# Kernel optimization log

Hardware: AMD Instinct MI355X
Metric: run time of the kernel (lower is better)

The kernel has to match this reference:

```python
import jax, jax.numpy as jnp
import numpy as np

# ---- module constants (from init_kwargs) ----
S = 524288            # number of env states (batch)
N_OBJ = 8             # 1 agent + 7 enemies
N_PROP = 6
AGENT_IDX = np.array([0])
ENEMY_IDX = np.array([1, 2, 3, 4, 5, 6, 7])
TYPE_OBJ = [AGENT_IDX, ENEMY_IDX]          # obj_type_indices per type name
TYPE_CODES = [(0, 1), (1, 0)]              # passed_obj_combs
PROP_CODES = np.array([0, 1])              # props
P_SATISFIED = np.array([True, True])       # p_satisfactions
EXIST_THRESH = 0.8


def setup_inputs() -> dict:
    key = jax.random.key(0)
    k1, = jax.random.split(key, 1)
    x = jax.random.uniform(k1, (S, N_OBJ, N_PROP), dtype=jnp.float32)
    action = jnp.array([1.0, 0.0, 1.0], dtype=jnp.float32)      # action_type
    mask = jnp.array([True, False])                              # action_mask
    pred_bounds = jnp.array([[0.0, 0.5], [0.1, 0.9]], dtype=jnp.float32)  # per-pred [min,max]
    return {"x": x, "action": action, "mask": mask, "pred_bounds": pred_bounds}


def _check_exists(x, mask):
    # faithful to check_exists: x[:, obj_type_indices, obj_indices] > 0.8, prod over objs
    agent_exist = jnp.all(x[:, AGENT_IDX, 0] > EXIST_THRESH, axis=-1)   # (S,)
    enemy_exist = jnp.all(x[:, ENEMY_IDX, 1] > EXIST_THRESH, axis=-1)   # (S,)
    obj_type_exists = jnp.stack([agent_exist, enemy_exist], axis=1)      # (S, 2)
    return jnp.all(mask[None, :] == obj_type_exists, axis=1)            # (S,)


def reference(x, action, mask, pred_bounds):
    exist_satisfy = _check_exists(x, mask)                 # (S,)
    action_norm = action / (action + 1e-20)                # value written to satisfied rows
    p_flags = jnp.asarray(P_SATISFIED)                     # (npred,)
    ap_list, pv_list = [], []
    for (t1, t2) in TYPE_CODES:
        o1, o2 = TYPE_OBJ[t1], TYPE_OBJ[t2]
        o1g, o2g = np.meshgrid(o1, o2, indexing="ij")      # all (obj_1, obj_2) pairs
        o1f, o2f = o1g.reshape(-1), o2g.reshape(-1)        # (P,)
        A = x[:, o1f[:, None], PROP_CODES[None, :]]        # (S, P, nprop)
        B = x[:, o2f[:, None], PROP_CODES[None, :]]
        d = jnp.abs(A - B)[..., None]                      # (S, P, nprop, 1)
        # pred.eval: within [min, max] parameter bound; p_values = evaluated distance
        sat = (d >= pred_bounds[:, 0]) & (d <= pred_bounds[:, 1])   # (S, P, nprop, npred)
        sat = jnp.where(p_flags, sat, True)                # unsatisfied preds -> all-true
        pv = jnp.where(p_flags, jnp.broadcast_to(d, sat.shape), 0.0)
        comb_sat = jnp.all(sat, axis=-1)                   # prod over preds   (S, P, nprop)
        satisfies = jnp.any(comb_sat, axis=(1, 2)) & exist_satisfy   # bool += then *= exist
        ap = jnp.where(satisfies[:, None], action_norm[None, :], 0.0)  # (S, n_actions)
        ap_list.append(ap)
        # p_spaces list order: obj pair -> prop -> pred, each entry (1, S)
        pv_list.append(jnp.transpose(pv, (1, 2, 3, 0)).reshape(-1, x.shape[0]))
    action_probs = jnp.stack(ap_list)   # (n_combs, S, n_actions)
    p_values = jnp.stack(pv_list)       # (n_combs, P*nprop*npred, S)
    return (action_probs, p_values)
```

## Files before the change

kernel.cpp:

```cpp
#include <hip/hip_runtime.h>


__global__ __launch_bounds__(256) void ump_kernel(
    const float* __restrict__ x,
    const float* __restrict__ action,
    const unsigned char* __restrict__ mask,
    const float* __restrict__ pred_bounds,
    float* __restrict__ out, int S)
{
    int s = blockIdx.x * blockDim.x + threadIdx.x;
    if (s >= S) return;

    const float* row = x + (size_t)s * 48;

    float2 a = *(const float2*)(row);

    const float lo0 = pred_bounds[0], hi0 = pred_bounds[1];
    const float lo1 = pred_bounds[2], hi1 = pred_bounds[3];

    float d[14];
    bool enemy_all = true;
    bool any_sat = false;
#pragma unroll
    for (int i = 0; i < 7; ++i) {
        float2 b = *(const float2*)(row + (i + 1) * 6);
        enemy_all = enemy_all && (b.y > 0.8f);
        float d0 = fabsf(a.x - b.x);
        float d1 = fabsf(a.y - b.y);
        d[2 * i]     = d0;
        d[2 * i + 1] = d1;
        bool s0 = (d0 >= lo0) && (d0 <= hi0) && (d0 >= lo1) && (d0 <= hi1);
        bool s1 = (d1 >= lo0) && (d1 <= hi0) && (d1 >= lo1) && (d1 <= hi1);
        any_sat = any_sat || s0 || s1;
    }

    bool agent_exist = a.x > 0.8f;
    bool m0 = mask[0] != 0;
    bool m1 = mask[1] != 0;
    bool exist     = (m0 == agent_exist) && (m1 == enemy_all);
    bool satisfies = exist && any_sat;

    float an0 = action[0] / (action[0] + 1e-20f);
    float an1 = action[1] / (action[1] + 1e-20f);
    float an2 = action[2] / (action[2] + 1e-20f);
    float v0 = satisfies ? an0 : 0.0f;
    float v1 = satisfies ? an1 : 0.0f;
    float v2 = satisfies ? an2 : 0.0f;

    size_t sl = (size_t)s;
    size_t Sl = (size_t)S;

    float* ap0 = out + sl * 3;
    ap0[0] = v0; ap0[1] = v1; ap0[2] = v2;
    float* ap1 = out + Sl * 3 + sl * 3;
    ap1[0] = v0; ap1[1] = v1; ap1[2] = v2;

    float* q = out + Sl * 6 + sl;
#pragma unroll
    for (int t = 0; t < 2; ++t) {
#pragma unroll
        for (int i = 0; i < 7; ++i) {
#pragma unroll
            for (int p = 0; p < 2; ++p) {
                float val = d[2 * i + p];
                q[0] = val; q += Sl;
                q[0] = val; q += Sl;
            }
        }
    }
}

extern "C" void kernel_launch(void* const* d_in, const int* in_sizes, int n_in,
                              void* d_out, int out_size, void* d_ws, size_t ws_size,
                              hipStream_t stream) {
    const float*         x           = (const float*)d_in[0];
    const float*         action      = (const float*)d_in[1];
    const unsigned char* mask        = (const unsigned char*)d_in[2];
    const float*         pred_bounds = (const float*)d_in[3];
    float* out = (float*)d_out;

    const int S = in_sizes[0] / 48;
    const int block = 256;
    const int grid = (S + block - 1) / block;
    ump_kernel<<<grid, block, 0, stream>>>(x, action, mask, pred_bounds, out, S);
}
```

Baseline: 214.7 us.

## Process four states per thread with vectorized nontemporal output stores

Each thread now handles four consecutive states, so the per-state distance values can be written as 128-bit vector stores along the S dimension, and the action-prob rows as 16-byte vector stores. All output stores use nontemporal hints to avoid cache pollution. The change cuts the number of store instructions, but input reads become strided across four rows per thread and the thread count drops by four, which lowers occupancy and latency hiding. It also assumes S is a multiple of 4.

```diff
diff --git a/kernel.cpp b/kernel.cpp
--- a/kernel.cpp
+++ b/kernel.cpp
@@ -1,5 +1,7 @@
 #include <hip/hip_runtime.h>
 
+
+typedef float v4f __attribute__((ext_vector_type(4)));
 
 __global__ __launch_bounds__(256) void ump_kernel(
     const float* __restrict__ x,
@@ -8,65 +10,83 @@
     const float* __restrict__ pred_bounds,
     float* __restrict__ out, int S)
 {
-    int s = blockIdx.x * blockDim.x + threadIdx.x;
-    if (s >= S) return;
+    int t = blockIdx.x * blockDim.x + threadIdx.x;
+    int s0 = t * 4;
+    if (s0 >= S) return;
 
-    const float* row = x + (size_t)s * 48;
-
-    float2 a = *(const float2*)(row);
+    const size_t Sl = (size_t)S;
+    const float* row0 = x + (size_t)s0 * 48;
 
     const float lo0 = pred_bounds[0], hi0 = pred_bounds[1];
     const float lo1 = pred_bounds[2], hi1 = pred_bounds[3];
 
-    float d[14];
-    bool enemy_all = true;
-    bool any_sat = false;
+    float2 a[4];
+#pragma unroll
+    for (int r = 0; r < 4; ++r)
+        a[r] = *(const float2*)(row0 + r * 48);
+
+    bool enemy_all[4] = {true, true, true, true};
+    bool any_sat[4]   = {false, false, false, false};
+
+    float* pv = out + Sl * 6 + s0;
+
 #pragma unroll
     for (int i = 0; i < 7; ++i) {
-        float2 b = *(const float2*)(row + (i + 1) * 6);
-        enemy_all = enemy_all && (b.y > 0.8f);
-        float d0 = fabsf(a.x - b.x);
-        float d1 = fabsf(a.y - b.y);
-        d[2 * i]     = d0;
-        d[2 * i + 1] = d1;
-        bool s0 = (d0 >= lo0) && (d0 <= hi0) && (d0 >= lo1) && (d0 <= hi1);
-        bool s1 = (d1 >= lo0) && (d1 <= hi0) && (d1 >= lo1) && (d1 <= hi1);
-        any_sat = any_sat || s0 || s1;
+        float2 b[4];
+#pragma unroll
+        for (int r = 0; r < 4; ++r)
+            b[r] = *(const float2*)(row0 + r * 48 + (i + 1) * 6);
+
+        v4f d0, d1;
+#pragma unroll
+        for (int r = 0; r < 4; ++r) {
+            float e0 = fabsf(a[r].x - b[r].x);
+            float e1 = fabsf(a[r].y - b[r].y);
+            d0[r] = e0;
+            d1[r] = e1;
+            enemy_all[r] = enemy_all[r] && (b[r].y > 0.8f);
+            bool s0b = (e0 >= lo0) && (e0 <= hi0) && (e0 >= lo1) && (e0 <= hi1);
+            bool s1b = (e1 >= lo0) && (e1 <= hi0) && (e1 >= lo1) && (e1 <= hi1);
+            any_sat[r] = any_sat[r] || s0b || s1b;
+        }
+
+        float* q = pv + (size_t)(4 * i) * Sl;
+        __builtin_nontemporal_store(d0, (v4f*)(q));
+        __builtin_nontemporal_store(d0, (v4f*)(q + Sl));
+        __builtin_nontemporal_store(d1, (v4f*)(q + 2 * Sl));
+        __builtin_nontemporal_store(d1, (v4f*)(q + 3 * Sl));
+        float* q2 = q + 28 * Sl;
+        __builtin_nontemporal_store(d0, (v4f*)(q2));
+        __builtin_nontemporal_store(d0, (v4f*)(q2 + Sl));
+        __builtin_nontemporal_store(d1, (v4f*)(q2 + 2 * Sl));
+        __builtin_nontemporal_store(d1, (v4f*)(q2 + 3 * Sl));
     }
 
-    bool agent_exist = a.x > 0.8f;
     bool m0 = mask[0] != 0;
     bool m1 = mask[1] != 0;
-    bool exist     = (m0 == agent_exist) && (m1 == enemy_all);
-    bool satisfies = exist && any_sat;
-
     float an0 = action[0] / (action[0] + 1e-20f);
     float an1 = action[1] / (action[1] + 1e-20f);
     float an2 = action[2] / (action[2] + 1e-20f);
-    float v0 = satisfies ? an0 : 0.0f;
-    float v1 = satisfies ? an1 : 0.0f;
-    float v2 = satisfies ? an2 : 0.0f;
 
-    size_t sl = (size_t)s;
-    size_t Sl = (size_t)S;
-
-    float* ap0 = out + sl * 3;
-    ap0[0] = v0; ap0[1] = v1; ap0[2] = v2;
-    float* ap1 = out + Sl * 3 + sl * 3;
-    ap1[0] = v0; ap1[1] = v1; ap1[2] = v2;
-
-    float* q = out + Sl * 6 + sl;
+    v4f ap[3];
 #pragma unroll
-    for (int t = 0; t < 2; ++t) {
+    for (int r = 0; r < 4; ++r) {
+        bool agent_exist = a[r].x > 0.8f;
+        bool exist = (m0 == agent_exist) && (m1 == enemy_all[r]);
+        bool sat   = exist && any_sat[r];
+        float v0 = sat ? an0 : 0.0f;
+        float v1 = sat ? an1 : 0.0f;
+        float v2 = sat ? an2 : 0.0f;
+        ((float*)ap)[3 * r]     = v0;
+        ((float*)ap)[3 * r + 1] = v1;
+        ((float*)ap)[3 * r + 2] = v2;
+    }
+    float* ap0 = out + (size_t)s0 * 3;
+    float* ap1 = out + Sl * 3 + (size_t)s0 * 3;
 #pragma unroll
-        for (int i = 0; i < 7; ++i) {
-#pragma unroll
-            for (int p = 0; p < 2; ++p) {
-                float val = d[2 * i + p];
-                q[0] = val; q += Sl;
-                q[0] = val; q += Sl;
-            }
-        }
+    for (int j = 0; j < 3; ++j) {
+        __builtin_nontemporal_store(ap[j], (v4f*)ap0 + j);
+        __builtin_nontemporal_store(ap[j], (v4f*)ap1 + j);
     }
 }
 
@@ -80,7 +100,8 @@
     float* out = (float*)d_out;
 
     const int S = in_sizes[0] / 48;
+    const int threads = S / 4;
     const int block = 256;
-    const int grid = (S + block - 1) / block;
+    const int grid = (threads + block - 1) / block;
     ump_kernel<<<grid, block, 0, stream>>>(x, action, mask, pred_bounds, out, S);
 }
```

Measured after the change: 225.4 us. +5.0%, slower.
